# Kernel tuning notes

Hardware: AMD Instinct MI355X
Metric: run time of the kernel (lower is better)

Reference implementation:

```python
import jax, jax.numpy as jnp
import numpy as np

STEP_SIZE = 0.01  # init kwarg step_size

def _quad_grad(A, b, x):
    # grad of per-node quadratic: 2*A_n @ x_n + b_n ; shapes [N,D,D],[N,D],[N,D]
    return 2.0 * jnp.einsum('nij,nj->ni', A, x) + b

def setup_inputs() -> dict:
    key = jax.random.key(0)
    kA, kb, kx, ke = jax.random.split(key, 4)
    N, D, E = 20000, 64, 320000
    A = jax.random.normal(kA, (N, D, D), dtype=jnp.float32)
    b = jax.random.normal(kb, (N, D), dtype=jnp.float32)
    x = jax.random.normal(kx, (N, D), dtype=jnp.float32)
    edge_index = jax.random.randint(ke, (2, E), 0, N, dtype=jnp.int64)
    return {"A": A, "b": b, "x": x, "edge_index": edge_index, "num_layers": 10}

def reference(A, b, x, edge_index, num_layers):
    N, D = x.shape
    src, dst = edge_index[0], edge_index[1]
    # push-sum column-stochastic mixing weights: 1/out_degree incl. self-loop
    deg = jnp.ones((N,), x.dtype).at[src].add(1.0)
    inv_deg = (1.0 / deg)[:, None]  # [N,1]

    def mix(z):  # z: [N,F]
        msg = z[src] * inv_deg[src]  # gather + weight
        agg = jax.ops.segment_sum(msg, dst, num_segments=N)
        return agg + z * inv_deg  # self-loop term

    y = _quad_grad(A, b, x)
    u = x
    v = jnp.ones((N, 1), x.dtype)
    x0 = x
    x1 = x0
    for _ in range(num_layers):
        u = mix(u - STEP_SIZE * y)          # conv on u
        v = mix(v)                           # conv on v (push-sum weight)
        x1 = u * (1.0 / v)                   # inv_v * u
        g1 = _quad_grad(A, b, x1)
        g0 = _quad_grad(A, b, x0)
        y = mix(y) + g1 - g0                 # conv on y + gradient tracking
        x0 = x1
    comm_cost = jnp.asarray(3 * num_layers * src.shape[0], dtype=jnp.int64)
    return x1, comm_cost
```

## Files before the change

kernel.cpp:

```cpp
#include <hip/hip_runtime.h>
#include <hip/hip_bf16.h>
#include <hip/hip_fp16.h>

#define STEP 0.01f
#define D 64
#define NUM_LAYERS 10

union H4 { uint2 u; __half h[4]; };
union H8 { uint4 u; __half2 h2[4]; __half h[8]; };


__global__ void k_setup(float* __restrict__ degf, int* __restrict__ degd, int N) {
    int n = blockIdx.x * blockDim.x + threadIdx.x;
    if (n < N) { degf[n] = 1.0f; degd[n] = 0; }
}

__global__ void k_deg2(const int* __restrict__ ei, float* __restrict__ degf,
                       int* __restrict__ degd, int E) {
    int e = blockIdx.x * blockDim.x + threadIdx.x;
    if (e < E) {
        unsafeAtomicAdd(&degf[ei[e]], 1.0f);
        atomicAdd(&degd[ei[E + e]], 1);
    }
}

__global__ __launch_bounds__(1024) void k_scan(
        const int* __restrict__ degd, const float* __restrict__ degf,
        int* __restrict__ row_ptr, int* __restrict__ cursor,
        float* __restrict__ invdeg, int N, int E) {
    __shared__ int part[1024];
    int tid = threadIdx.x;
    int chunk = (N + 1023) / 1024;
    int lo = tid * chunk, hi = min(lo + chunk, N);
    int s = 0;
    for (int i = lo; i < hi; ++i) s += degd[i];
    part[tid] = s;
    __syncthreads();
    for (int off = 1; off < 1024; off <<= 1) {
        int v = (tid >= off) ? part[tid - off] : 0;
        __syncthreads();
        part[tid] += v;
        __syncthreads();
    }
    int base = (tid == 0) ? 0 : part[tid - 1];
    for (int i = lo; i < hi; ++i) {
        row_ptr[i] = base;
        cursor[i] = base;
        base += degd[i];
        invdeg[i] = 1.0f / degf[i];
    }
    if (tid == 1023) row_ptr[N] = E;
}

__global__ void k_scatter(const int* __restrict__ ei, int* __restrict__ cursor,
                          int* __restrict__ col, int E) {
    int e = blockIdx.x * blockDim.x + threadIdx.x;
    if (e < E) {
        int pos = atomicAdd(&cursor[ei[E + e]], 1);
        col[pos] = ei[e];
    }
}


__global__ __launch_bounds__(256) void k_init(
        const float* __restrict__ A, const float* __restrict__ b,
        const float* __restrict__ x, const float* __restrict__ invdeg,
        __half* __restrict__ Ah, __half2* __restrict__ msg,
        float* __restrict__ vw, float* __restrict__ x0, int N) {
    __shared__ __align__(16) float sx[D];
    __shared__ float syv[D];
    int n = blockIdx.x, t = threadIdx.x;
    int lane = t & 63, w = t >> 6, colgrp = lane & 15;
    if (t < D) sx[t] = x[(size_t)n * D + t];
    __syncthreads();
    const float* An = A + (size_t)n * D * D;
    __half* Ahn = Ah + (size_t)n * D * D;
    float4 xr = ((const float4*)sx)[colgrp];
    int rbase = w * 16 + (lane >> 4);
#pragma unroll
    for (int g = 0; g < 4; ++g) {
        int row = rbase + g * 4;
        float4 a = ((const float4*)(An + (size_t)row * D))[colgrp];
        H4 pk;
        pk.h[0] = __float2half(a.x);
        pk.h[1] = __float2half(a.y);
        pk.h[2] = __float2half(a.z);
        pk.h[3] = __float2half(a.w);
        ((uint2*)(Ahn + (size_t)row * D))[colgrp] = pk.u;
        float p = a.x * xr.x + a.y * xr.y + a.z * xr.z + a.w * xr.w;
        p += __shfl_xor(p, 1);
        p += __shfl_xor(p, 2);
        p += __shfl_xor(p, 4);
        p += __shfl_xor(p, 8);
        if (colgrp == 0) syv[row] = 2.0f * p + b[(size_t)n * D + row];
    }
    __syncthreads();
    if (t < D) {
        float wd = invdeg[n];
        float xv = sx[t];
        float yv = syv[t];
        msg[(size_t)n * D + t] = __floats2half2_rn((xv - STEP * yv) * wd, yv * wd);
        x0[(size_t)n * D + t] = xv;
        if (t == 0) vw[n] = wd;
    }
}


__global__ __launch_bounds__(256) void k_layer(
        const __half* __restrict__ Ah,
        const int* __restrict__ row_ptr, const int* __restrict__ col,
        const __half2* __restrict__ msg, const float* __restrict__ vw,
        const float* __restrict__ invdeg,
        __half2* __restrict__ msgn, float* __restrict__ vwn,
        float* __restrict__ x0, float* __restrict__ xout,
        int last_idx, float comm, int N) {
    __shared__ float su[4][D];
    __shared__ float sy[4][D];
    __shared__ float sv[4];
    __shared__ __align__(16) float sdx[D];
    __shared__ float sun[D];
    __shared__ float sytot[D];

    int n = blockIdx.x, t = threadIdx.x;
    int lane = t & 63, w = t >> 6;
    int j = lane >> 4, q4 = lane & 15;

    int rs = row_ptr[n], re = row_ptr[n + 1];
    const uint4* Ahp = (const uint4*)(Ah + (size_t)n * D * D);
    H8 a0, a1;
    a0.u = Ahp[t];
    a1.u = Ahp[256 + t];
    float invd = invdeg[n];
    float2 self = {0.0f, 0.0f};
    float x0v = 0.0f, vwself = 0.0f;
    if (w == 0) {
        size_t off = (size_t)n * D + lane;
        self = __half22float2(msg[off]);
        x0v = x0[off];
        vwself = vw[n];
    }

    float4 au = {0.f, 0.f, 0.f, 0.f}, ay = {0.f, 0.f, 0.f, 0.f};
    float av = 0.0f;
    for (int base = rs + w * 4; base < re; base += 16) {
        int e = base + j;
        if (e < re) {
            int s = col[e];
            H8 m;
            m.u = ((const uint4*)(msg + (size_t)s * D))[q4];
            float2 f0 = __half22float2(m.h2[0]);
            float2 f1 = __half22float2(m.h2[1]);
            float2 f2 = __half22float2(m.h2[2]);
            float2 f3 = __half22float2(m.h2[3]);
            au.x += f0.x; ay.x += f0.y;
            au.y += f1.x; ay.y += f1.y;
            au.z += f2.x; ay.z += f2.y;
            au.w += f3.x; ay.w += f3.y;
            if (q4 == 0) av += vw[s];
        }
    }
    au.x += __shfl_xor(au.x, 16); au.y += __shfl_xor(au.y, 16);
    au.z += __shfl_xor(au.z, 16); au.w += __shfl_xor(au.w, 16);
    au.x += __shfl_xor(au.x, 32); au.y += __shfl_xor(au.y, 32);
    au.z += __shfl_xor(au.z, 32); au.w += __shfl_xor(au.w, 32);
    ay.x += __shfl_xor(ay.x, 16); ay.y += __shfl_xor(ay.y, 16);
    ay.z += __shfl_xor(ay.z, 16); ay.w += __shfl_xor(ay.w, 16);
    ay.x += __shfl_xor(ay.x, 32); ay.y += __shfl_xor(ay.y, 32);
    ay.z += __shfl_xor(ay.z, 32); ay.w += __shfl_xor(ay.w, 32);
    av += __shfl_xor(av, 16);
    av += __shfl_xor(av, 32);
    if (j == 0) {
        ((float4*)su[w])[q4] = au;
        ((float4*)sy[w])[q4] = ay;
        if (q4 == 0) sv[w] = av;
    }
    __syncthreads();

    if (w == 0) {
        size_t off = (size_t)n * D + lane;
        float ut = su[0][lane] + su[1][lane] + su[2][lane] + su[3][lane] + self.x;
        float yt = sy[0][lane] + sy[1][lane] + sy[2][lane] + sy[3][lane] + self.y;
        float vt = sv[0] + sv[1] + sv[2] + sv[3] + vwself;
        float x1 = ut / vt;
        sdx[lane] = x1 - x0v;
        x0[off] = x1;
        if (xout) xout[off] = x1;
        sun[lane] = ut;
        sytot[lane] = yt;
        if (lane == 0) vwn[n] = vt * invd;
        if (xout && n == 0 && lane == 0) xout[last_idx] = comm;
    }
    __syncthreads();

    {
        int cb = (t & 7) * 8;
        int r0 = t >> 3;
        float p0 = 0.0f, p1 = 0.0f;
#pragma unroll
        for (int jj = 0; jj < 8; ++jj) {
            float dv = sdx[cb + jj];
            p0 += __half2float(a0.h[jj]) * dv;
            p1 += __half2float(a1.h[jj]) * dv;
        }
        p0 += __shfl_xor(p0, 1); p1 += __shfl_xor(p1, 1);
        p0 += __shfl_xor(p0, 2); p1 += __shfl_xor(p1, 2);
        p0 += __shfl_xor(p0, 4); p1 += __shfl_xor(p1, 4);
        if ((lane & 7) == 0) {
            float yn0 = sytot[r0]      + 2.0f * p0;
            float yn1 = sytot[32 + r0] + 2.0f * p1;
            msgn[(size_t)n * D + r0] =
                __floats2half2_rn((sun[r0] - STEP * yn0) * invd, yn0 * invd);
            msgn[(size_t)n * D + 32 + r0] =
                __floats2half2_rn((sun[32 + r0] - STEP * yn1) * invd, yn1 * invd);
        }
    }
}


extern "C" void kernel_launch(void* const* d_in, const int* in_sizes, int n_in,
                              void* d_out, int out_size, void* d_ws, size_t ws_size,
                              hipStream_t stream) {
    const float* A  = (const float*)d_in[0];
    const float* b  = (const float*)d_in[1];
    const float* x  = (const float*)d_in[2];
    const int*   ei = (const int*)d_in[3];

    const int N = in_sizes[1] / D;
    const int E = in_sizes[3] / 2;
    const size_t ND = (size_t)N * D;

    char* ws = (char*)d_ws;
    __half* Ah = (__half*)ws;
    __half2* msg0 = (__half2*)(ws + ND * D * sizeof(__half));
    __half2* msg1 = msg0 + ND;
    float* x0   = (float*)(msg1 + ND);
    float* vw0  = x0 + ND;
    float* vw1  = vw0 + N;
    float* invdeg = vw1 + N;
    float* degf = invdeg + N;
    int* degd    = (int*)(degf + N);
    int* row_ptr = degd + N;
    int* cursor  = row_ptr + N + 4;
    int* col     = cursor + N;

    k_setup<<<(N + 255) / 256, 256, 0, stream>>>(degf, degd, N);
    k_deg2<<<(E + 255) / 256, 256, 0, stream>>>(ei, degf, degd, E);
    k_scan<<<1, 1024, 0, stream>>>(degd, degf, row_ptr, cursor, invdeg, N, E);
    k_scatter<<<(E + 255) / 256, 256, 0, stream>>>(ei, cursor, col, E);
    k_init<<<N, 256, 0, stream>>>(A, b, x, invdeg, Ah, msg0, vw0, x0, N);

    float comm = (float)(3 * NUM_LAYERS * E);
    __half2 *mc = msg0, *mn = msg1;
    float *vc = vw0, *vn = vw1;
    for (int l = 0; l < NUM_LAYERS; ++l) {
        float* xout = (l == NUM_LAYERS - 1) ? (float*)d_out : nullptr;
        k_layer<<<N, 256, 0, stream>>>(Ah, row_ptr, col, mc, vc, invdeg,
                                       mn, vn, x0, xout, out_size - 1, comm, N);
        __half2* tm = mc; mc = mn; mn = tm;
        float* tv = vc; vc = vn; vn = tv;
    }
}
```

Measured before the change: 978.6 us.

## Map one node per wavefront in layer kernel, eliminating shared memory and barriers

The layer kernel now assigns one node to each 64-lane wavefront, with four nodes per block, instead of one node per 256-thread block. Edge aggregation, the x1 update and the A·dx matvec are all done inside the wave using shuffles, so the shared memory and both __syncthreads are gone. Each lane holds eight 16-byte chunks of A, and the edge loop processes two edges per lane-group per iteration for more memory-level parallelism. The costs are more registers per thread, high-degree nodes now being gathered by one wave instead of four, and a fast reciprocal in place of the exact division.

```diff
diff --git a/kernel.cpp b/kernel.cpp
--- a/kernel.cpp
+++ b/kernel.cpp
@@ -114,50 +114,58 @@
         __half2* __restrict__ msgn, float* __restrict__ vwn,
         float* __restrict__ x0, float* __restrict__ xout,
         int last_idx, float comm, int N) {
-    __shared__ float su[4][D];
-    __shared__ float sy[4][D];
-    __shared__ float sv[4];
-    __shared__ __align__(16) float sdx[D];
-    __shared__ float sun[D];
-    __shared__ float sytot[D];
-
-    int n = blockIdx.x, t = threadIdx.x;
+    int t = threadIdx.x;
     int lane = t & 63, w = t >> 6;
+    int n = blockIdx.x * 4 + w;
+    if (n >= N) return;
+
     int j = lane >> 4, q4 = lane & 15;
-
     int rs = row_ptr[n], re = row_ptr[n + 1];
-    const uint4* Ahp = (const uint4*)(Ah + (size_t)n * D * D);
-    H8 a0, a1;
-    a0.u = Ahp[t];
-    a1.u = Ahp[256 + t];
+
+    const uint4* Ap = (const uint4*)(Ah + (size_t)n * D * D);
+    uint4 a[8];
+#pragma unroll
+    for (int k = 0; k < 8; ++k) a[k] = Ap[lane + 64 * k];
+
+    size_t off = (size_t)n * D + lane;
+    float2 msf = __half22float2(msg[off]);
+    float x0v = x0[off];
+    float vwn_self = vw[n];
     float invd = invdeg[n];
-    float2 self = {0.0f, 0.0f};
-    float x0v = 0.0f, vwself = 0.0f;
-    if (w == 0) {
-        size_t off = (size_t)n * D + lane;
-        self = __half22float2(msg[off]);
-        x0v = x0[off];
-        vwself = vw[n];
-    }
 
     float4 au = {0.f, 0.f, 0.f, 0.f}, ay = {0.f, 0.f, 0.f, 0.f};
     float av = 0.0f;
-    for (int base = rs + w * 4; base < re; base += 16) {
-        int e = base + j;
-        if (e < re) {
-            int s = col[e];
-            H8 m;
-            m.u = ((const uint4*)(msg + (size_t)s * D))[q4];
-            float2 f0 = __half22float2(m.h2[0]);
-            float2 f1 = __half22float2(m.h2[1]);
-            float2 f2 = __half22float2(m.h2[2]);
-            float2 f3 = __half22float2(m.h2[3]);
-            au.x += f0.x; ay.x += f0.y;
-            au.y += f1.x; ay.y += f1.y;
-            au.z += f2.x; ay.z += f2.y;
-            au.w += f3.x; ay.w += f3.y;
-            if (q4 == 0) av += vw[s];
-        }
+    for (int base = rs; base < re; base += 8) {
+        int e0 = base + (j << 1), e1 = e0 + 1;
+        bool b0 = e0 < re, b1 = e1 < re;
+        int s0 = 0, s1 = 0;
+        if (b0) s0 = col[e0];
+        if (b1) s1 = col[e1];
+        H8 m0, m1;
+        m0.u = make_uint4(0u, 0u, 0u, 0u);
+        m1.u = make_uint4(0u, 0u, 0u, 0u);
+        float w0 = 0.f, w1 = 0.f;
+        if (b0) m0.u = ((const uint4*)(msg + (size_t)s0 * D))[q4];
+        if (b1) m1.u = ((const uint4*)(msg + (size_t)s1 * D))[q4];
+        if (b0 && q4 == 0) w0 = vw[s0];
+        if (b1 && q4 == 0) w1 = vw[s1];
+        float2 f0 = __half22float2(m0.h2[0]);
+        float2 f1 = __half22float2(m0.h2[1]);
+        float2 f2 = __half22float2(m0.h2[2]);
+        float2 f3 = __half22float2(m0.h2[3]);
+        au.x += f0.x; ay.x += f0.y;
+        au.y += f1.x; ay.y += f1.y;
+        au.z += f2.x; ay.z += f2.y;
+        au.w += f3.x; ay.w += f3.y;
+        f0 = __half22float2(m1.h2[0]);
+        f1 = __half22float2(m1.h2[1]);
+        f2 = __half22float2(m1.h2[2]);
+        f3 = __half22float2(m1.h2[3]);
+        au.x += f0.x; ay.x += f0.y;
+        au.y += f1.x; ay.y += f1.y;
+        au.z += f2.x; ay.z += f2.y;
+        au.w += f3.x; ay.w += f3.y;
+        av += w0 + w1;
     }
     au.x += __shfl_xor(au.x, 16); au.y += __shfl_xor(au.y, 16);
     au.z += __shfl_xor(au.z, 16); au.w += __shfl_xor(au.w, 16);
@@ -169,51 +177,56 @@
     ay.z += __shfl_xor(ay.z, 32); ay.w += __shfl_xor(ay.w, 32);
     av += __shfl_xor(av, 16);
     av += __shfl_xor(av, 32);
-    if (j == 0) {
-        ((float4*)su[w])[q4] = au;
-        ((float4*)sy[w])[q4] = ay;
-        if (q4 == 0) sv[w] = av;
-    }
-    __syncthreads();
-
-    if (w == 0) {
-        size_t off = (size_t)n * D + lane;
-        float ut = su[0][lane] + su[1][lane] + su[2][lane] + su[3][lane] + self.x;
-        float yt = sy[0][lane] + sy[1][lane] + sy[2][lane] + sy[3][lane] + self.y;
-        float vt = sv[0] + sv[1] + sv[2] + sv[3] + vwself;
-        float x1 = ut / vt;
-        sdx[lane] = x1 - x0v;
-        x0[off] = x1;
-        if (xout) xout[off] = x1;
-        sun[lane] = ut;
-        sytot[lane] = yt;
-        if (lane == 0) vwn[n] = vt * invd;
-        if (xout && n == 0 && lane == 0) xout[last_idx] = comm;
-    }
-    __syncthreads();
-
-    {
-        int cb = (t & 7) * 8;
-        int r0 = t >> 3;
-        float p0 = 0.0f, p1 = 0.0f;
-#pragma unroll
-        for (int jj = 0; jj < 8; ++jj) {
-            float dv = sdx[cb + jj];
-            p0 += __half2float(a0.h[jj]) * dv;
-            p1 += __half2float(a1.h[jj]) * dv;
-        }
-        p0 += __shfl_xor(p0, 1); p1 += __shfl_xor(p1, 1);
-        p0 += __shfl_xor(p0, 2); p1 += __shfl_xor(p1, 2);
-        p0 += __shfl_xor(p0, 4); p1 += __shfl_xor(p1, 4);
-        if ((lane & 7) == 0) {
-            float yn0 = sytot[r0]      + 2.0f * p0;
-            float yn1 = sytot[32 + r0] + 2.0f * p1;
-            msgn[(size_t)n * D + r0] =
-                __floats2half2_rn((sun[r0] - STEP * yn0) * invd, yn0 * invd);
-            msgn[(size_t)n * D + 32 + r0] =
-                __floats2half2_rn((sun[32 + r0] - STEP * yn1) * invd, yn1 * invd);
-        }
-    }
+    av = __shfl(av, 0);
+
+    int src = lane >> 2, c = lane & 3;
+    float ua = __shfl(au.x, src), ub = __shfl(au.y, src),
+          uc = __shfl(au.z, src), ud = __shfl(au.w, src);
+    float ya = __shfl(ay.x, src), yb = __shfl(ay.y, src),
+          yc = __shfl(ay.z, src), yd = __shfl(ay.w, src);
+    float ut = (c & 2) ? ((c & 1) ? ud : uc) : ((c & 1) ? ub : ua);
+    float yt = (c & 2) ? ((c & 1) ? yd : yc) : ((c & 1) ? yb : ya);
+    ut += msf.x;
+    yt += msf.y;
+
+    float vt = av + vwn_self;
+    float rvt = __builtin_amdgcn_rcpf(vt);
+    float x1 = ut * rvt;
+    float dx = x1 - x0v;
+    x0[off] = x1;
+    if (xout) xout[off] = x1;
+    if (lane == 0) vwn[n] = vt * invd;
+    if (xout && n == 0 && lane == 0) xout[last_idx] = comm;
+
+    int cb = (lane & 7) * 8;
+    float dxv[8];
+#pragma unroll
+    for (int jj = 0; jj < 8; ++jj) dxv[jj] = __shfl(dx, cb + jj);
+
+    float pk[8];
+#pragma unroll
+    for (int k = 0; k < 8; ++k) {
+        H8 aa; aa.u = a[k];
+        float p = 0.f;
+#pragma unroll
+        for (int jj = 0; jj < 8; ++jj)
+            p += __half2float(aa.h[jj]) * dxv[jj];
+        p += __shfl_xor(p, 1);
+        p += __shfl_xor(p, 2);
+        p += __shfl_xor(p, 4);
+        pk[k] = p;
+    }
+    int srcg = (lane & 7) * 8;
+    float pr[8];
+#pragma unroll
+    for (int k = 0; k < 8; ++k) pr[k] = __shfl(pk[k], srcg);
+    int kk = lane >> 3;
+    float prow = (kk & 4) ? ((kk & 2) ? ((kk & 1) ? pr[7] : pr[6])
+                                      : ((kk & 1) ? pr[5] : pr[4]))
+                          : ((kk & 2) ? ((kk & 1) ? pr[3] : pr[2])
+                                      : ((kk & 1) ? pr[1] : pr[0]));
+    float yn = yt + 2.0f * prow;
+    msgn[off] = __floats2half2_rn((ut - STEP * yn) * invd, yn * invd);
 }
 
 
@@ -254,8 +267,8 @@
     float *vc = vw0, *vn = vw1;
     for (int l = 0; l < NUM_LAYERS; ++l) {
         float* xout = (l == NUM_LAYERS - 1) ? (float*)d_out : nullptr;
-        k_layer<<<N, 256, 0, stream>>>(Ah, row_ptr, col, mc, vc, invdeg,
-                                       mn, vn, x0, xout, out_size - 1, comm, N);
+        k_layer<<<(N + 3) / 4, 256, 0, stream>>>(Ah, row_ptr, col, mc, vc, invdeg,
+                                                 mn, vn, x0, xout, out_size - 1, comm, N);
         __half2* tm = mc; mc = mn; mn = tm;
         float* tv = vc; vc = vn; vn = tv;
     }
```

New measurement: 960.6 us. Within noise of the previous version (-1.8%).
